# Performance work log

Hardware: AMD Instinct MI355X
Metric: run time of the kernel (lower is better)

## Reference

```python
import math
import jax, jax.numpy as jnp
import numpy as np

CLIP = 1.0e4
DT = 0.1
JITTER = 1.0e-5
MIN_SCALE = 1.0e-4
MAX_TRIES = 8


def _san_vec(v):
    v = jnp.nan_to_num(v, nan=0.0, posinf=CLIP, neginf=-CLIP)
    return jnp.clip(v, -CLIP, CLIP)


def _san_mat(m):
    m = _san_vec(m)
    return 0.5 * (m + jnp.swapaxes(m, -1, -2))


def _softplus_inv(v):
    v = max(float(v), 1e-8)
    return v if v > 20.0 else math.log(math.expm1(v))


def _stable_inverse_logdet(M, base_jitter):
    # M: [..., 2, 2]; vectorized version of the torch retry loop: try
    # jitter * 10**k for k in 0..MAX_TRIES-1, take the first PD repair.
    eye = jnp.eye(2, dtype=M.dtype)
    cand = _san_mat(M)
    diag = jnp.diagonal(cand, axis1=-2, axis2=-1)            # [..., 2]
    diag_scale = jnp.maximum(jnp.mean(jnp.abs(diag), -1), 1.0)  # [...]
    j0 = max(base_jitter, 1e-6)
    jitters = j0 * (10.0 ** jnp.arange(MAX_TRIES, dtype=M.dtype))  # [K]
    rep = _san_mat(cand[..., None, :, :]
                   + (jitters[:, None, None] * diag_scale[..., None, None, None]) * eye)  # [..., K, 2, 2]
    chol = jnp.linalg.cholesky(rep)                           # NaN where not PD
    ok = jnp.all(jnp.isfinite(chol), axis=(-1, -2))           # [..., K]
    any_ok = jnp.any(ok, -1)                                  # [...]
    idx = jnp.argmax(ok, -1)                                  # first success
    take = lambda a: jnp.take_along_axis(a, idx[..., None, None, None], axis=-3)[..., 0, :, :]
    rep_s, chol_s = take(rep), take(chol)
    log_det = 2.0 * jnp.sum(jnp.log(jnp.diagonal(chol_s, axis1=-2, axis2=-1)), -1)
    inv_s = _san_mat(jnp.linalg.inv(rep_s))
    # fallback diagonal repair (jitter after full loop = j0 * 10**MAX_TRIES)
    jfin = j0 * 10.0 ** MAX_TRIES
    sd = jnp.nan_to_num(diag, nan=1.0, posinf=CLIP, neginf=1.0)
    sd = jnp.maximum(jnp.abs(sd), jfin * diag_scale[..., None] + 1e-4)
    rep_fb = _san_mat(sd[..., :, None] * eye + (jfin * diag_scale[..., None, None]) * eye)
    d_fb = jnp.maximum(jnp.diagonal(rep_fb, axis1=-2, axis2=-1), 1e-6)
    inv_fb = _san_mat((1.0 / d_fb)[..., :, None] * eye)
    ld_fb = jnp.sum(jnp.log(d_fb), -1)
    sel = any_ok[..., None, None]
    repaired = jnp.where(sel, rep_s, rep_fb)
    inverse = jnp.where(sel, inv_s, inv_fb)
    log_det = jnp.where(any_ok, log_det, ld_fb)
    log_det = jnp.nan_to_num(log_det, nan=0.0, posinf=20.0, neginf=-20.0)
    return repaired, inverse, log_det


def setup_inputs() -> dict:
    key = jax.random.key(0)
    k1, k2, k3 = jax.random.split(key, 3)
    T, C, S = 32, 2, 512
    means = jax.random.normal(k1, (T, C, 2), dtype=jnp.float32)
    covariances = jax.random.normal(k2, (T, C, 2, 2), dtype=jnp.float32)
    site_coords = jax.random.normal(k3, (S, 2), dtype=jnp.float32)
    raw = np.full((C, C), _softplus_inv(0.02), dtype=np.float32)
    np.fill_diagonal(raw, _softplus_inv(1.0))
    block_scale_raw = jnp.asarray(raw)
    mix = min(max(0.1, 1e-6), 1.0 - 1e-6)
    identity_mix_logit = jnp.asarray(math.log(mix / (1.0 - mix)), dtype=jnp.float32)
    return {"means": means, "covariances": covariances, "site_coords": site_coords,
            "block_scale_raw": block_scale_raw, "identity_mix_logit": identity_mix_logit}


def reference(means, covariances, site_coords, block_scale_raw, identity_mix_logit):
    T, C = means.shape[0], means.shape[1]
    S = site_coords.shape[0]
    eye2 = jnp.eye(2, dtype=jnp.float32)
    means = _san_vec(means)
    covs = _san_mat(covariances)
    lags = _san_vec(site_coords[:, None, :] - site_coords[None, :, :])   # [S, S, 2]
    scales = jax.nn.softplus(block_scale_raw) + MIN_SCALE                 # [C, C]
    mask = jnp.ones((C, C), dtype=jnp.float32)                            # allow_cross_component=True
    mix = jax.nn.sigmoid(identity_mix_logit)
    same = jnp.eye(C, dtype=bool)
    # drift / dispersion for all (t, i, j) blocks
    drift_same = DT * means[:, :, None, :]                                # mean_i, [T,C,1,2]
    drift_cross = DT * (means[:, :, None, :] - means[:, None, :, :])      # [T,C,C,2]
    drift = jnp.where(same[None, :, :, None], drift_same, drift_cross)
    rel_same = jnp.broadcast_to(covs[:, :, None], (T, C, C, 2, 2))        # cov_i
    rel_cross = covs[:, :, None] + covs[:, None, :]                       # cov_i + cov_j
    rel = jnp.where(same[None, :, :, None, None], rel_same, rel_cross)
    drift = _san_vec(drift)
    disp = _san_mat(eye2 + 2.0 * DT ** 2 * rel + JITTER * eye2)           # [T,C,C,2,2]
    repaired, inv_disp, log_det = _stable_inverse_logdet(disp, JITTER)
    # quadratic form over all site pairs
    centered = _san_vec(lags[None, None, None] - drift[:, :, :, None, None, :])  # [T,C,C,S,S,2]
    quad = jnp.einsum('tijabk,tijkl,tijabl->tijab', centered, inv_disp, centered)
    quad = jnp.clip(jnp.nan_to_num(quad, nan=0.0, posinf=60.0, neginf=0.0), 0.0, 60.0)
    exponent = jnp.clip(-0.5 * log_det[..., None, None] - quad, -60.0, 20.0)
    block = (mask * scales)[None, :, :, None, None] * jnp.exp(exponent)   # [T,C,C,S,S]
    block = jnp.nan_to_num(block, nan=0.0, posinf=0.0, neginf=0.0)
    # assemble [T, C*S, C*S] with component-major ordering
    kernel = jnp.transpose(block, (0, 1, 3, 2, 4)).reshape(T, C * S, C * S)
    trans = kernel / jnp.maximum(kernel.sum(-1, keepdims=True), JITTER)
    trans = jnp.nan_to_num(trans, nan=0.0, posinf=0.0, neginf=0.0)
    trans = trans / jnp.maximum(trans.sum(-1, keepdims=True), JITTER)
    I = jnp.eye(C * S, dtype=trans.dtype)
    trans = (1.0 - mix) * trans + mix * I
    trans = jnp.nan_to_num(trans, nan=0.0, posinf=0.0, neginf=0.0)
    trans = trans / jnp.maximum(trans.sum(-1, keepdims=True), JITTER)
    return trans, drift, repaired
```

## Files before the change

kernel.cpp:

```cpp
#include <hip/hip_runtime.h>
#include <math.h>

#define CLIPV 1.0e4f
#define DT 0.1f
#define JITTER 1.0e-5f
#define MIN_SCALE 1.0e-4f

typedef float __attribute__((ext_vector_type(4))) fx4;

__device__ __forceinline__ float sanv(float x) {
    if (__builtin_isnan(x)) return 0.0f;
    return fminf(fmaxf(x, -CLIPV), CLIPV);
}

__global__ void prep_kernel(const float* __restrict__ means,
                            const float* __restrict__ covs,
                            const float* __restrict__ bsr,
                            float* __restrict__ ws,
                            float* __restrict__ drift_out,
                            float* __restrict__ rep_out) {
    int idx = threadIdx.x;
    if (idx >= 128) return;
    int t = idx >> 2, i = (idx >> 1) & 1, j = idx & 1;

    float mi0 = sanv(means[(t * 2 + i) * 2 + 0]);
    float mi1 = sanv(means[(t * 2 + i) * 2 + 1]);
    float mj0 = sanv(means[(t * 2 + j) * 2 + 0]);
    float mj1 = sanv(means[(t * 2 + j) * 2 + 1]);

    float d0, d1;
    if (i == j) { d0 = DT * mi0; d1 = DT * mi1; }
    else        { d0 = DT * (mi0 - mj0); d1 = DT * (mi1 - mj1); }
    d0 = sanv(d0); d1 = sanv(d1);

    auto covsym = [&](int cc, float& a, float& b, float& d) {
        const float* p = covs + ((t * 2 + cc) * 4);
        float m00 = sanv(p[0]), m01 = sanv(p[1]), m10 = sanv(p[2]), m11 = sanv(p[3]);
        a = m00; b = 0.5f * (m01 + m10); d = m11;
    };
    float ra, rb, rd;
    covsym(i, ra, rb, rd);
    if (i != j) { float sa, sb, sd; covsym(j, sa, sb, sd); ra += sa; rb += sb; rd += sd; }

    const float c2 = 2.0f * DT * DT;
    float A = sanv(1.0f + c2 * ra + JITTER);
    float B = sanv(c2 * rb);
    float D = sanv(1.0f + c2 * rd + JITTER);

    float diag_scale = fmaxf(0.5f * (fabsf(A) + fabsf(D)), 1.0f);
    const float j0 = 1e-5f;
    float repA = 0.f, repB = 0.f, repD = 0.f;
    float invA = 0.f, invB = 0.f, invD = 0.f, logdet = 0.f;
    bool found = false;
    float jit = j0;
    for (int k = 0; k < 8; ++k) {
        float add = jit * diag_scale;
        float a = sanv(A + add), b = B, d = sanv(D + add);
        float det = a * d - b * b;
        if (a > 0.0f && det > 0.0f && __builtin_isfinite(det)) {
            repA = a; repB = b; repD = d;
            logdet = logf(det);
            float rdet = 1.0f / det;
            invA = sanv(d * rdet); invB = sanv(-b * rdet); invD = sanv(a * rdet);
            found = true;
            break;
        }
        jit *= 10.0f;
    }
    if (!found) {
        float jfin = j0 * 1.0e8f;
        float add = jfin * diag_scale;
        float sd0 = fmaxf(fabsf(A), add + 1e-4f);
        float sd1 = fmaxf(fabsf(D), add + 1e-4f);
        repA = sanv(sd0 + add); repB = 0.0f; repD = sanv(sd1 + add);
        float dfb0 = fmaxf(repA, 1e-6f), dfb1 = fmaxf(repD, 1e-6f);
        invA = sanv(1.0f / dfb0); invB = 0.0f; invD = sanv(1.0f / dfb1);
        logdet = logf(dfb0) + logf(dfb1);
    }
    if (__builtin_isnan(logdet)) logdet = 0.0f;
    else if (__builtin_isinf(logdet)) logdet = logdet > 0.0f ? 20.0f : -20.0f;

    float x = bsr[i * 2 + j];
    float sp = fmaxf(x, 0.0f) + log1pf(expf(-fabsf(x)));
    float scale = sp + MIN_SCALE;

    float* W = ws + idx * 8;
    W[0] = invA; W[1] = invB; W[2] = invD; W[3] = logdet;
    W[4] = d0;   W[5] = d1;   W[6] = scale; W[7] = 0.0f;

    drift_out[idx * 2 + 0] = d0;
    drift_out[idx * 2 + 1] = d1;
    rep_out[idx * 4 + 0] = repA;
    rep_out[idx * 4 + 1] = repB;
    rep_out[idx * 4 + 2] = repB;
    rep_out[idx * 4 + 3] = repD;
}

__global__ __launch_bounds__(256) void row2_kernel(
        const float* __restrict__ site,
        const float* __restrict__ ws,
        const float* __restrict__ mix_logit_p,
        float* __restrict__ out) {
    int bid  = blockIdx.x;
    int tid  = threadIdx.x;
    int lane = tid & 63;
    int wid  = tid >> 6;

    int t  = bid >> 7;
    int rb = ((bid & 127) << 3) + (wid << 1);
    int i  = rb >> 9;

    const float* P0 = ws + (((t * 2 + i) * 2 + 0) * 8);
    const float* P1 = ws + (((t * 2 + i) * 2 + 1) * 8);
    float m000 = P0[0], tm010 = 2.0f * P0[1], m110 = P0[2];
    float nldh0 = -0.5f * P0[3];
    float dr00 = P0[4], dr10 = P0[5], sc0 = P0[6];
    float m001 = P1[0], tm011 = 2.0f * P1[1], m111 = P1[2];
    float nldh1 = -0.5f * P1[3];
    float dr01 = P1[4], dr11 = P1[5], sc1 = P1[6];
    float E0 = __expf(nldh0), E1 = __expf(nldh1);

    float mix = 1.0f / (1.0f + __expf(-mix_logit_p[0]));

#pragma unroll 1
    for (int rr = 0; rr < 2; ++rr) {
        int arow = rb + rr;
        int a = arow & 511;
        float sa0 = site[a * 2 + 0];
        float sa1 = site[a * 2 + 1];
        float ra00 = sa0 - dr00, ra10 = sa1 - dr10;
        float ra01 = sa0 - dr01, ra11 = sa1 - dr11;

        float e[16];
        float p0 = 0.0f, p1 = 0.0f;
#pragma unroll
        for (int q = 0; q < 4; ++q) {
            int g0 = q * 256 + lane * 4;
            int b0 = g0 & 511;
            float m00, tm01, m11, ra0, ra1;
            if (q < 2) { m00 = m000; tm01 = tm010; m11 = m110; ra0 = ra00; ra1 = ra10; }
            else       { m00 = m001; tm01 = tm011; m11 = m111; ra0 = ra01; ra1 = ra11; }

            float4 sb01 = *(const float4*)(site + b0 * 2);
            float4 sb23 = *(const float4*)(site + b0 * 2 + 4);
            float bx[4] = {sb01.x, sb01.z, sb23.x, sb23.z};
            float by[4] = {sb01.y, sb01.w, sb23.y, sb23.w};

            float acc = 0.0f;
#pragma unroll
            for (int m = 0; m < 4; ++m) {
                float v0 = ra0 - bx[m];
                float v1 = ra1 - by[m];
                float quad = m00 * (v0 * v0) + tm01 * (v0 * v1) + m11 * (v1 * v1);
                float ev = __expf(-quad);
                e[q * 4 + m] = ev;
                acc += ev;
            }
            if (q < 2) p0 += acc; else p1 += acc;
        }

        float partial = sc0 * E0 * p0 + sc1 * E1 * p1;
#pragma unroll
        for (int off = 32; off; off >>= 1)
            partial += __shfl_xor(partial, off, 64);
        float s = partial;

        float r1 = fmaxf(s, JITTER);
        float s1 = s / r1;
        float r2 = fmaxf(s1, JITTER);
        float s2 = s1 / r2;
        float s3 = (1.0f - mix) * s2 + mix;
        float r3 = fmaxf(s3, JITTER);
        float f = (1.0f - mix) / (r1 * r2 * r3);
        float diagadd = mix / r3;
        float f0 = f * sc0 * E0, f1 = f * sc1 * E1;

        int diagcol = i * 512 + a;
        float* orow = out + ((size_t)t * 1024 + (size_t)arow) * 1024;

#pragma unroll
        for (int q = 0; q < 4; ++q) {
            int g0 = q * 256 + lane * 4;
            float ff = (q < 2) ? f0 : f1;
            float vv[4];
#pragma unroll
            for (int m = 0; m < 4; ++m) {
                float v = e[q * 4 + m] * ff;
                if ((g0 + m) == diagcol) v += diagadd;
                vv[m] = v;
            }
            fx4 o = {vv[0], vv[1], vv[2], vv[3]};
            __builtin_nontemporal_store(o, (fx4*)(orow + g0));
        }
    }
}

extern "C" void kernel_launch(void* const* d_in, const int* in_sizes, int n_in,
                              void* d_out, int out_size, void* d_ws, size_t ws_size,
                              hipStream_t stream) {
    const float* means = (const float*)d_in[0];
    const float* covs  = (const float*)d_in[1];
    const float* site  = (const float*)d_in[2];
    const float* bsr   = (const float*)d_in[3];
    const float* mixl  = (const float*)d_in[4];
    float* out = (float*)d_out;
    float* ws  = (float*)d_ws;

    const size_t TRANS = 32ull * 1024 * 1024;
    float* drift_out = out + TRANS;
    float* rep_out   = out + TRANS + 256;

    prep_kernel<<<1, 128, 0, stream>>>(means, covs, bsr, ws, drift_out, rep_out);
    row2_kernel<<<4096, 256, 0, stream>>>(site, ws, mixl, out);
}
```

Before: 35.90 us.

## Process four rows per wave and expand quadratic form with precomputed column terms

Each wave now handles four output rows instead of two, and the column site coordinates are loaded once and kept in registers. The quadratic form is expanded algebraically into a per-row constant, per-row linear coefficients and a per-column precomputed quadratic term, so each element costs two FMAs plus an add instead of the full difference-and-square. This cuts ALU work and repeated site loads, but raises register pressure and halves the grid size, and the expanded form may lose some floating-point precision through cancellation.

New measurement: 36.13 us. About the same (+0.7%).

```diff
diff --git a/kernel.cpp b/kernel.cpp
--- a/kernel.cpp
+++ b/kernel.cpp
@@ -96,7 +96,7 @@
     rep_out[idx * 4 + 3] = repD;
 }
 
-__global__ __launch_bounds__(256) void row2_kernel(
+__global__ __launch_bounds__(256) void row4_kernel(
         const float* __restrict__ site,
         const float* __restrict__ ws,
         const float* __restrict__ mix_logit_p,
@@ -106,60 +106,84 @@
     int lane = tid & 63;
     int wid  = tid >> 6;
 
-    int t  = bid >> 7;
-    int rb = ((bid & 127) << 3) + (wid << 1);
-    int i  = rb >> 9;
+    int t    = bid >> 6;
+    int rblk = ((bid & 63) << 4) + (wid << 2);
+    int i    = rblk >> 9;
 
     const float* P0 = ws + (((t * 2 + i) * 2 + 0) * 8);
     const float* P1 = ws + (((t * 2 + i) * 2 + 1) * 8);
     float m000 = P0[0], tm010 = 2.0f * P0[1], m110 = P0[2];
-    float nldh0 = -0.5f * P0[3];
-    float dr00 = P0[4], dr10 = P0[5], sc0 = P0[6];
+    float dr00 = P0[4], dr10 = P0[5];
+    float sE0  = P0[6] * __expf(-0.5f * P0[3]);
     float m001 = P1[0], tm011 = 2.0f * P1[1], m111 = P1[2];
-    float nldh1 = -0.5f * P1[3];
-    float dr01 = P1[4], dr11 = P1[5], sc1 = P1[6];
-    float E0 = __expf(nldh0), E1 = __expf(nldh1);
+    float dr01 = P1[4], dr11 = P1[5];
+    float sE1  = P1[6] * __expf(-0.5f * P1[3]);
 
     float mix = 1.0f / (1.0f + __expf(-mix_logit_p[0]));
 
+    float bx[16], by[16], Qb[16];
+#pragma unroll
+    for (int q = 0; q < 4; ++q) {
+        int b0 = (q * 256 + lane * 4) & 511;
+        float4 sb01 = *(const float4*)(site + b0 * 2);
+        float4 sb23 = *(const float4*)(site + b0 * 2 + 4);
+        bx[q * 4 + 0] = sb01.x; by[q * 4 + 0] = sb01.y;
+        bx[q * 4 + 1] = sb01.z; by[q * 4 + 1] = sb01.w;
+        bx[q * 4 + 2] = sb23.x; by[q * 4 + 2] = sb23.y;
+        bx[q * 4 + 3] = sb23.z; by[q * 4 + 3] = sb23.w;
+        float m00 = (q < 2) ? m000 : m001;
+        float tm01 = (q < 2) ? tm010 : tm011;
+        float m11 = (q < 2) ? m110 : m111;
+#pragma unroll
+        for (int m = 0; m < 4; ++m) {
+            int k = q * 4 + m;
+            Qb[k] = m00 * bx[k] * bx[k] + tm01 * bx[k] * by[k] + m11 * by[k] * by[k];
+        }
+    }
+
+    int abase = rblk & 511;
+    float4 sa01 = *(const float4*)(site + abase * 2);
+    float4 sa23 = *(const float4*)(site + abase * 2 + 4);
+    float sax[4] = {sa01.x, sa01.z, sa23.x, sa23.z};
+    float say[4] = {sa01.y, sa01.w, sa23.y, sa23.w};
+
 #pragma unroll 1
-    for (int rr = 0; rr < 2; ++rr) {
-        int arow = rb + rr;
-        int a = arow & 511;
-        float sa0 = site[a * 2 + 0];
-        float sa1 = site[a * 2 + 1];
-        float ra00 = sa0 - dr00, ra10 = sa1 - dr10;
-        float ra01 = sa0 - dr01, ra11 = sa1 - dr11;
+    for (int rr = 0; rr < 4; ++rr) {
+        int arow = rblk + rr;
+        int a = abase + rr;
+        float sa0 = sax[rr], sa1 = say[rr];
+
+        float ra0 = sa0 - dr00, ra1 = sa1 - dr10;
+        float c00 = m000 * ra0 * ra0 + tm010 * ra0 * ra1 + m110 * ra1 * ra1;
+        float c10 = -(2.0f * m000 * ra0 + tm010 * ra1);
+        float c20 = -(tm010 * ra0 + 2.0f * m110 * ra1);
+        float rb0 = sa0 - dr01, rb1 = sa1 - dr11;
+        float c01 = m001 * rb0 * rb0 + tm011 * rb0 * rb1 + m111 * rb1 * rb1;
+        float c11 = -(2.0f * m001 * rb0 + tm011 * rb1);
+        float c21 = -(tm011 * rb0 + 2.0f * m111 * rb1);
 
         float e[16];
         float p0 = 0.0f, p1 = 0.0f;
 #pragma unroll
         for (int q = 0; q < 4; ++q) {
-            int g0 = q * 256 + lane * 4;
-            int b0 = g0 & 511;
-            float m00, tm01, m11, ra0, ra1;
-            if (q < 2) { m00 = m000; tm01 = tm010; m11 = m110; ra0 = ra00; ra1 = ra10; }
-            else       { m00 = m001; tm01 = tm011; m11 = m111; ra0 = ra01; ra1 = ra11; }
-
-            float4 sb01 = *(const float4*)(site + b0 * 2);
-            float4 sb23 = *(const float4*)(site + b0 * 2 + 4);
-            float bx[4] = {sb01.x, sb01.z, sb23.x, sb23.z};
-            float by[4] = {sb01.y, sb01.w, sb23.y, sb23.w};
-
+            float c0 = (q < 2) ? c00 : c01;
+            float c1 = (q < 2) ? c10 : c11;
+            float c2 = (q < 2) ? c20 : c21;
             float acc = 0.0f;
 #pragma unroll
             for (int m = 0; m < 4; ++m) {
-                float v0 = ra0 - bx[m];
-                float v1 = ra1 - by[m];
-                float quad = m00 * (v0 * v0) + tm01 * (v0 * v1) + m11 * (v1 * v1);
-                float ev = __expf(-quad);
-                e[q * 4 + m] = ev;
+                int k = q * 4 + m;
+                float qd = c0 + Qb[k];
+                qd = fmaf(c1, bx[k], qd);
+                qd = fmaf(c2, by[k], qd);
+                float ev = __expf(-qd);
+                e[k] = ev;
                 acc += ev;
             }
             if (q < 2) p0 += acc; else p1 += acc;
         }
 
-        float partial = sc0 * E0 * p0 + sc1 * E1 * p1;
+        float partial = sE0 * p0 + sE1 * p1;
 #pragma unroll
         for (int off = 32; off; off >>= 1)
             partial += __shfl_xor(partial, off, 64);
@@ -173,7 +197,7 @@
         float r3 = fmaxf(s3, JITTER);
         float f = (1.0f - mix) / (r1 * r2 * r3);
         float diagadd = mix / r3;
-        float f0 = f * sc0 * E0, f1 = f * sc1 * E1;
+        float f0 = f * sE0, f1 = f * sE1;
 
         int diagcol = i * 512 + a;
         float* orow = out + ((size_t)t * 1024 + (size_t)arow) * 1024;
@@ -211,5 +235,5 @@
     float* rep_out   = out + TRANS + 256;
 
     prep_kernel<<<1, 128, 0, stream>>>(means, covs, bsr, ws, drift_out, rep_out);
-    row2_kernel<<<4096, 256, 0, stream>>>(site, ws, mixl, out);
-}
+    row4_kernel<<<2048, 256, 0, stream>>>(site, ws, mixl, out);
+}
```
